# Performance work log

Hardware: AMD Instinct MI355X
Metric: run time of the kernel (lower is better)

Reference implementation:

```python
import jax, jax.numpy as jnp
import numpy as np
from jax import lax

BATCH, SEQ_LEN, INPUT_DIM, OUTPUT_DIM = 64, 1000, 512, 512
KERNEL_WIDTH = 5  # context [-2, 2] with full_context=True -> range(-2, 3)


def setup_inputs() -> dict:
    key = jax.random.key(0)
    k1, k2, k3 = jax.random.split(key, 3)
    stdv = 1.0 / np.sqrt(INPUT_DIM)
    x = jax.random.normal(k1, (BATCH, SEQ_LEN, INPUT_DIM), dtype=jnp.float32)
    kernel = stdv * jax.random.normal(k2, (OUTPUT_DIM, INPUT_DIM, KERNEL_WIDTH), dtype=jnp.float32)
    bias = stdv * jax.random.normal(k3, (OUTPUT_DIM,), dtype=jnp.float32)
    return {"x": x, "kernel": kernel, "bias": bias}


def reference(x, kernel, bias):
    # x: [B, T, C_in] -> [B, C_in, T]
    xt = jnp.transpose(x, (0, 2, 1))
    # Contiguous full context == single VALID conv over time.
    # Original loop: for each valid step i, gather x[:, :, context+i] and conv1d,
    # which for context=range(-2,3) is exactly this strided convolution.
    out = lax.conv_general_dilated(
        xt, kernel,
        window_strides=(1,), padding="VALID",
        dimension_numbers=("NCH", "OIH", "NCH"),
    )  # [B, C_out, T - K + 1]
    out = out + bias[None, :, None]
    # ReLU then transpose back to [B, T_valid, C_out]
    return jnp.transpose(jax.nn.relu(out), (0, 2, 1))
```

## Files before the change

### kernel.cpp

```cpp
#include <hip/hip_runtime.h>
#include <hip/hip_bf16.h>


#define BATCH 64
#define SEQ   1000
#define CIN   512
#define COUT  512
#define TOUT  996
#define KTOT  2560
#define MTOT  63744
#define NKT   40
#define MT    249
#define NT    2
#define NWG   (MT*NT)

typedef __bf16 bf16x8 __attribute__((ext_vector_type(8)));
typedef float  f32x4  __attribute__((ext_vector_type(4)));

__device__ __forceinline__ void gload_lds16(const void* g, void* l) {
  __builtin_amdgcn_global_load_lds(
      (const __attribute__((address_space(1))) void*)g,
      (__attribute__((address_space(3))) void*)l, 16, 0, 0);
}

#define BAR()    __builtin_amdgcn_s_barrier()
#define VM12()   asm volatile("s_waitcnt vmcnt(12)" ::: "memory")
#define VM8()    asm volatile("s_waitcnt vmcnt(8)"  ::: "memory")
#define VM4()    asm volatile("s_waitcnt vmcnt(4)"  ::: "memory")
#define PRIO(x)  __builtin_amdgcn_s_setprio(x)
#define SCHED0() __builtin_amdgcn_sched_barrier(0)
#define MFMA(d, x, y) d = __builtin_amdgcn_mfma_f32_16x16x32_bf16(x, y, d, 0, 0, 0)

__global__ void cvt_x_kernel(const float* __restrict__ x, __bf16* __restrict__ xb, int n) {
  int i = (blockIdx.x * blockDim.x + threadIdx.x) * 8;
  if (i >= n) return;
  float4 f0 = *(const float4*)(x + i);
  float4 f1 = *(const float4*)(x + i + 4);
  bf16x8 v;
  v[0] = (__bf16)f0.x; v[1] = (__bf16)f0.y; v[2] = (__bf16)f0.z; v[3] = (__bf16)f0.w;
  v[4] = (__bf16)f1.x; v[5] = (__bf16)f1.y; v[6] = (__bf16)f1.z; v[7] = (__bf16)f1.w;
  *(bf16x8*)(xb + i) = v;
}

__global__ void cvt_w_kernel(const float* __restrict__ k, __bf16* __restrict__ wt) {
  int idx = blockIdx.x * blockDim.x + threadIdx.x;
  if (idx >= 80 * 32 * 512) return;
  int j  = idx & 7;
  int l  = (idx >> 3) & 63;
  int t1 = idx >> 9;
  int ob = t1 & 31;
  int ks = t1 >> 5;
  int o  = ob * 16 + (l & 15);
  int kk = ks * 32 + ((l >> 4) & 3) * 8 + j;
  int c  = kk & 511, kw = kk >> 9;
  wt[idx] = (__bf16)k[(o * CIN + c) * 5 + kw];
}

#define STAGE(buf, kt) do { \
    char* d_ = (char*)Ab + ((buf) << 15); \
    gload_lds16(Xb + offA0 + (kt) * 64, d_ + dof0); \
    gload_lds16(Xb + offA1 + (kt) * 64, d_ + dof1); \
    gload_lds16(Xb + offA2 + (kt) * 64, d_ + dof2); \
    gload_lds16(Xb + offA3 + (kt) * 64, d_ + dof3); } while (0)

#define LOADB(bn, Tn) do { \
    const char* p_ = Wglob + (size_t)(Tn) * 65536; \
    bn[0][0] = *(const bf16x8*)(p_ +     0); bn[0][1] = *(const bf16x8*)(p_ + 32768); \
    bn[1][0] = *(const bf16x8*)(p_ +  1024); bn[1][1] = *(const bf16x8*)(p_ + 33792); \
    bn[2][0] = *(const bf16x8*)(p_ +  2048); bn[2][1] = *(const bf16x8*)(p_ + 34816); \
    bn[3][0] = *(const bf16x8*)(p_ +  3072); bn[3][1] = *(const bf16x8*)(p_ + 35840); } while (0)

#define TILE(T, bc, bn) do { \
    const bool s1_ = (T) + 1 < NKT, s2_ = (T) + 2 < NKT; \
    if (s1_) LOADB(bn, (T) + 1); \
    if (s2_) STAGE(((T) + 2) & 3, (T) + 2); \
    const char* Ac_ = Aw + (((T) & 3) << 15); \
    bf16x8 a_[4][2]; \
    _Pragma("unroll") \
    for (int mi = 0; mi < 4; ++mi) { \
      a_[mi][0] = *(const bf16x8*)(Ac_ + mi * 2048 + off0); \
      a_[mi][1] = *(const bf16x8*)(Ac_ + mi * 2048 + off1); \
    } \
    PRIO(1); \
    _Pragma("unroll") \
    for (int mi = 0; mi < 4; ++mi) \
      _Pragma("unroll") \
      for (int nj = 0; nj < 4; ++nj) { \
        MFMA(acc[mi][nj], a_[mi][0], bc[nj][0]); \
        MFMA(acc[mi][nj], a_[mi][1], bc[nj][1]); \
      } \
    PRIO(0); \
    _Pragma("unroll") \
    for (int mi = 0; mi < 4; ++mi) { \
      a_[mi][0] = *(const bf16x8*)(Ac_ + (mi + 4) * 2048 + off0); \
      a_[mi][1] = *(const bf16x8*)(Ac_ + (mi + 4) * 2048 + off1); \
    } \
    PRIO(1); \
    _Pragma("unroll") \
    for (int mi = 0; mi < 4; ++mi) \
      _Pragma("unroll") \
      for (int nj = 0; nj < 4; ++nj) { \
        MFMA(acc[mi + 4][nj], a_[mi][0], bc[nj][0]); \
        MFMA(acc[mi + 4][nj], a_[mi][1], bc[nj][1]); \
      } \
    PRIO(0); \
    SCHED0(); \
    if (s2_) { VM12(); } else if (s1_) { VM8(); } \
    if (s1_) BAR(); \
  } while (0)

__global__ __launch_bounds__(512, 2)
void tdnn_gemm_kernel(const __bf16* __restrict__ Xb, const __bf16* __restrict__ Wt2,
                      const float* __restrict__ bias, float* __restrict__ out) {
  __shared__ __bf16 Ab[4][256][64];

  const int tid  = threadIdx.x;
  const int wave = tid >> 6;
  const int lane = tid & 63;
  const int wr = wave >> 2;
  const int wc = wave & 3;

  int bid = blockIdx.x;
  int xcd = bid & 7, jj = bid >> 3;
  const int q = NWG >> 3, r = NWG & 7;
  int swz = (xcd < r ? xcd * (q + 1) : r * (q + 1) + (xcd - r) * q) + jj;
  const int m0 = (swz >> 1) * 256;
  const int n0 = (swz & 1) * 256;

  int offA0, offA1, offA2, offA3, dof0, dof1, dof2, dof3;
  {
    int o16, row, ce, m, b, tt;
#define MKOFF(l, A, D) \
    o16 = (l) * 512 + tid; row = o16 >> 3; \
    ce  = ((((o16 & 7) << 4) ^ ((row & 7) << 4)) >> 1); \
    D   = o16 * 16; \
    m = m0 + row; b = m / TOUT; tt = m - b * TOUT; \
    A = (b * SEQ + tt) * CIN + ce;
    MKOFF(0, offA0, dof0)
    MKOFF(1, offA1, dof1)
    MKOFF(2, offA2, dof2)
    MKOFF(3, offA3, dof3)
#undef MKOFF
  }

  const int frow = lane & 15;
  const int fkb  = (lane >> 4) << 4;
  const int xorv = (frow & 7) << 4;
  const int off0 = fkb ^ xorv;
  const int off1 = (64 + fkb) ^ xorv;
  const char* Aw = (const char*)Ab + (wr * 128 + frow) * 128;

  const int obW = (n0 >> 4) + wc * 4;
  const char* Wglob = (const char*)Wt2 + obW * 1024 + lane * 16;

  f32x4 acc[8][4];
  const f32x4 z = {0.f, 0.f, 0.f, 0.f};
#pragma unroll
  for (int i = 0; i < 8; i++)
#pragma unroll
    for (int j = 0; j < 4; j++) acc[i][j] = z;

  bf16x8 bA[4][2], bB[4][2];

  LOADB(bA, 0);
  STAGE(0, 0);
  STAGE(1, 1);
  VM4();
  BAR();

  for (int T = 0; T < NKT; T += 2) {
    TILE(T,     bA, bB);
    TILE(T + 1, bB, bA);
  }

  const int ccol = lane & 15;
  const int crow = (lane >> 4) * 4;
  float bv[4];
#pragma unroll
  for (int nj = 0; nj < 4; ++nj)
    bv[nj] = bias[n0 + wc * 64 + nj * 16 + ccol];

#pragma unroll
  for (int mi = 0; mi < 8; ++mi) {
    const int mrow = m0 + wr * 128 + mi * 16 + crow;
#pragma unroll
    for (int nj = 0; nj < 4; ++nj) {
      const int ocol = n0 + wc * 64 + nj * 16 + ccol;
#pragma unroll
      for (int j = 0; j < 4; ++j) {
        float v = acc[mi][nj][j] + bv[nj];
        v = v > 0.f ? v : 0.f;
        out[(size_t)(mrow + j) * COUT + ocol] = v;
      }
    }
  }
}

extern "C" void kernel_launch(void* const* d_in, const int* in_sizes, int n_in,
                              void* d_out, int out_size, void* d_ws, size_t ws_size,
                              hipStream_t stream) {
  const float* x      = (const float*)d_in[0];
  const float* kernel = (const float*)d_in[1];
  const float* bias   = (const float*)d_in[2];
  float* out          = (float*)d_out;

  __bf16* xb  = (__bf16*)d_ws;
  __bf16* wt2 = (__bf16*)((char*)d_ws + (size_t)BATCH * SEQ * CIN * 2);

  const int nx = BATCH * SEQ * CIN;
  cvt_x_kernel<<<nx / 8 / 256, 256, 0, stream>>>(x, xb, nx);
  cvt_w_kernel<<<(80 * 32 * 512 + 255) / 256, 256, 0, stream>>>(kernel, wt2);
  tdnn_gemm_kernel<<<NWG, 512, 0, stream>>>(xb, wt2, bias, out);
}
```

Before: 201.1 us.

## Stage weights through LDS and split each K-tile into barrier-synced quadrants

Weights are now converted to a plain row-major [COUT][KTOT] bf16 layout and staged into LDS with direct global-to-LDS loads, replacing the earlier per-lane register prefetch from a fragment-packed layout. The A buffer drops from four stages to two, and a two-stage B buffer is added. Each K-tile's 8x4 MFMA block is split into four quadrants, with LDS reads, async stages and barriers interleaved between them in a ping-pong schedule. The aim is to cut per-wave global B traffic and VGPR pressure and to spread memory issue across the compute phases. The cost is many more barriers per tile and a shallower prefetch depth.

```diff
diff --git a/kernel.cpp b/kernel.cpp
--- a/kernel.cpp
+++ b/kernel.cpp
@@ -24,11 +24,11 @@
 }
 
 #define BAR()    __builtin_amdgcn_s_barrier()
-#define VM12()   asm volatile("s_waitcnt vmcnt(12)" ::: "memory")
-#define VM8()    asm volatile("s_waitcnt vmcnt(8)"  ::: "memory")
-#define VM4()    asm volatile("s_waitcnt vmcnt(4)"  ::: "memory")
+#define VM6()    asm volatile("s_waitcnt vmcnt(6)" ::: "memory")
+#define VM0()    asm volatile("s_waitcnt vmcnt(0)" ::: "memory")
+#define LGKM0()  asm volatile("s_waitcnt lgkmcnt(0)" ::: "memory")
+#define LGKM8()  asm volatile("s_waitcnt lgkmcnt(8)" ::: "memory")
 #define PRIO(x)  __builtin_amdgcn_s_setprio(x)
-#define SCHED0() __builtin_amdgcn_sched_barrier(0)
 #define MFMA(d, x, y) d = __builtin_amdgcn_mfma_f32_16x16x32_bf16(x, y, d, 0, 0, 0)
 
 __global__ void cvt_x_kernel(const float* __restrict__ x, __bf16* __restrict__ xb, int n) {
@@ -44,75 +44,50 @@
 
 __global__ void cvt_w_kernel(const float* __restrict__ k, __bf16* __restrict__ wt) {
   int idx = blockIdx.x * blockDim.x + threadIdx.x;
-  if (idx >= 80 * 32 * 512) return;
-  int j  = idx & 7;
-  int l  = (idx >> 3) & 63;
-  int t1 = idx >> 9;
-  int ob = t1 & 31;
-  int ks = t1 >> 5;
-  int o  = ob * 16 + (l & 15);
-  int kk = ks * 32 + ((l >> 4) & 3) * 8 + j;
-  int c  = kk & 511, kw = kk >> 9;
+  if (idx >= COUT * KTOT) return;
+  int o  = idx / KTOT;
+  int r  = idx - o * KTOT;
+  int kw = r >> 9;
+  int c  = r & 511;
   wt[idx] = (__bf16)k[(o * CIN + c) * 5 + kw];
 }
 
-#define STAGE(buf, kt) do { \
+#define STAGE_AH(buf, h, kt) do { \
     char* d_ = (char*)Ab + ((buf) << 15); \
-    gload_lds16(Xb + offA0 + (kt) * 64, d_ + dof0); \
-    gload_lds16(Xb + offA1 + (kt) * 64, d_ + dof1); \
-    gload_lds16(Xb + offA2 + (kt) * 64, d_ + dof2); \
-    gload_lds16(Xb + offA3 + (kt) * 64, d_ + dof3); } while (0)
-
-#define LOADB(bn, Tn) do { \
-    const char* p_ = Wglob + (size_t)(Tn) * 65536; \
-    bn[0][0] = *(const bf16x8*)(p_ +     0); bn[0][1] = *(const bf16x8*)(p_ + 32768); \
-    bn[1][0] = *(const bf16x8*)(p_ +  1024); bn[1][1] = *(const bf16x8*)(p_ + 33792); \
-    bn[2][0] = *(const bf16x8*)(p_ +  2048); bn[2][1] = *(const bf16x8*)(p_ + 34816); \
-    bn[3][0] = *(const bf16x8*)(p_ +  3072); bn[3][1] = *(const bf16x8*)(p_ + 35840); } while (0)
-
-#define TILE(T, bc, bn) do { \
-    const bool s1_ = (T) + 1 < NKT, s2_ = (T) + 2 < NKT; \
-    if (s1_) LOADB(bn, (T) + 1); \
-    if (s2_) STAGE(((T) + 2) & 3, (T) + 2); \
-    const char* Ac_ = Aw + (((T) & 3) << 15); \
-    bf16x8 a_[4][2]; \
+    gload_lds16(Xb + offA##h##0 + (kt) * 64, d_ + dstA##h##0); \
+    gload_lds16(Xb + offA##h##1 + (kt) * 64, d_ + dstA##h##1); } while (0)
+#define STAGE_BH(buf, h, kt) do { \
+    char* d_ = (char*)Bb + ((buf) << 15); \
+    gload_lds16(Wt + offB##h##0 + (kt) * 64, d_ + dstB##h##0); \
+    gload_lds16(Wt + offB##h##1 + (kt) * 64, d_ + dstB##h##1); } while (0)
+
+#define RDA4(dst, base, mi0) do { \
     _Pragma("unroll") \
-    for (int mi = 0; mi < 4; ++mi) { \
-      a_[mi][0] = *(const bf16x8*)(Ac_ + mi * 2048 + off0); \
-      a_[mi][1] = *(const bf16x8*)(Ac_ + mi * 2048 + off1); \
-    } \
+    for (int mi_ = 0; mi_ < 4; ++mi_) { \
+      dst[mi_][0] = *(const bf16x8*)((base) + ((mi0) + mi_) * 2048 + off0); \
+      dst[mi_][1] = *(const bf16x8*)((base) + ((mi0) + mi_) * 2048 + off1); } } while (0)
+#define RDB2(dst, base, nj0) do { \
+    _Pragma("unroll") \
+    for (int nj_ = 0; nj_ < 2; ++nj_) { \
+      dst[nj_][0] = *(const bf16x8*)((base) + ((nj0) + nj_) * 2048 + off0); \
+      dst[nj_][1] = *(const bf16x8*)((base) + ((nj0) + nj_) * 2048 + off1); } } while (0)
+
+#define QUAD(r0, c0, AF, BF) do { \
     PRIO(1); \
     _Pragma("unroll") \
-    for (int mi = 0; mi < 4; ++mi) \
+    for (int mi_ = 0; mi_ < 4; ++mi_) \
       _Pragma("unroll") \
-      for (int nj = 0; nj < 4; ++nj) { \
-        MFMA(acc[mi][nj], a_[mi][0], bc[nj][0]); \
-        MFMA(acc[mi][nj], a_[mi][1], bc[nj][1]); \
+      for (int nj_ = 0; nj_ < 2; ++nj_) { \
+        MFMA(acc[(r0) + mi_][(c0) + nj_], AF[mi_][0], BF[nj_][0]); \
+        MFMA(acc[(r0) + mi_][(c0) + nj_], AF[mi_][1], BF[nj_][1]); \
       } \
-    PRIO(0); \
-    _Pragma("unroll") \
-    for (int mi = 0; mi < 4; ++mi) { \
-      a_[mi][0] = *(const bf16x8*)(Ac_ + (mi + 4) * 2048 + off0); \
-      a_[mi][1] = *(const bf16x8*)(Ac_ + (mi + 4) * 2048 + off1); \
-    } \
-    PRIO(1); \
-    _Pragma("unroll") \
-    for (int mi = 0; mi < 4; ++mi) \
-      _Pragma("unroll") \
-      for (int nj = 0; nj < 4; ++nj) { \
-        MFMA(acc[mi + 4][nj], a_[mi][0], bc[nj][0]); \
-        MFMA(acc[mi + 4][nj], a_[mi][1], bc[nj][1]); \
-      } \
-    PRIO(0); \
-    SCHED0(); \
-    if (s2_) { VM12(); } else if (s1_) { VM8(); } \
-    if (s1_) BAR(); \
-  } while (0)
+    PRIO(0); } while (0)
 
 __global__ __launch_bounds__(512, 2)
-void tdnn_gemm_kernel(const __bf16* __restrict__ Xb, const __bf16* __restrict__ Wt2,
+void tdnn_gemm_kernel(const __bf16* __restrict__ Xb, const __bf16* __restrict__ Wt,
                       const float* __restrict__ bias, float* __restrict__ out) {
-  __shared__ __bf16 Ab[4][256][64];
+  __shared__ __bf16 Ab[2][256][64];
+  __shared__ __bf16 Bb[2][256][64];
 
   const int tid  = threadIdx.x;
   const int wave = tid >> 6;
@@ -127,20 +102,33 @@
   const int m0 = (swz >> 1) * 256;
   const int n0 = (swz & 1) * 256;
 
-  int offA0, offA1, offA2, offA3, dof0, dof1, dof2, dof3;
+  const int tq = tid >> 3;
+  const int t8 = tid & 7;
+  const int ce = (t8 ^ (tq & 7)) << 3;
+
+  int offA00, offA01, offA10, offA11, dstA00, dstA01, dstA10, dstA11;
+  int offB00, offB01, offB10, offB11, dstB00, dstB01, dstB10, dstB11;
   {
-    int o16, row, ce, m, b, tt;
-#define MKOFF(l, A, D) \
-    o16 = (l) * 512 + tid; row = o16 >> 3; \
-    ce  = ((((o16 & 7) << 4) ^ ((row & 7) << 4)) >> 1); \
-    D   = o16 * 16; \
-    m = m0 + row; b = m / TOUT; tt = m - b * TOUT; \
-    A = (b * SEQ + tt) * CIN + ce;
-    MKOFF(0, offA0, dof0)
-    MKOFF(1, offA1, dof1)
-    MKOFF(2, offA2, dof2)
-    MKOFF(3, offA3, dof3)
-#undef MKOFF
+    int rr, m, b, tt;
+#define MKA(h, l, A, D) \
+    rr = (h) * 64 + (l) * 128 + tq; \
+    m = m0 + rr; b = m / TOUT; tt = m - b * TOUT; \
+    A = (b * SEQ + tt) * CIN + ce; \
+    D = rr * 128 + (t8 << 4);
+    MKA(0, 0, offA00, dstA00)
+    MKA(0, 1, offA01, dstA01)
+    MKA(1, 0, offA10, dstA10)
+    MKA(1, 1, offA11, dstA11)
+#undef MKA
+#define MKB(h, l, B, D) \
+    rr = (h) * 32 + ((l) * 2 + (tid >> 8)) * 64 + (tq & 31); \
+    B = (n0 + rr) * KTOT + ce; \
+    D = rr * 128 + (t8 << 4);
+    MKB(0, 0, offB00, dstB00)
+    MKB(0, 1, offB01, dstB01)
+    MKB(1, 0, offB10, dstB10)
+    MKB(1, 1, offB11, dstB11)
+#undef MKB
   }
 
   const int frow = lane & 15;
@@ -148,10 +136,8 @@
   const int xorv = (frow & 7) << 4;
   const int off0 = fkb ^ xorv;
   const int off1 = (64 + fkb) ^ xorv;
-  const char* Aw = (const char*)Ab + (wr * 128 + frow) * 128;
-
-  const int obW = (n0 >> 4) + wc * 4;
-  const char* Wglob = (const char*)Wt2 + obW * 1024 + lane * 16;
+  const char* Ab0 = (const char*)Ab + (wr * 128 + frow) * 128;
+  const char* Bb0 = (const char*)Bb + (wc * 64 + frow) * 128;
 
   f32x4 acc[8][4];
   const f32x4 z = {0.f, 0.f, 0.f, 0.f};
@@ -160,17 +146,69 @@
 #pragma unroll
     for (int j = 0; j < 4; j++) acc[i][j] = z;
 
-  bf16x8 bA[4][2], bB[4][2];
-
-  LOADB(bA, 0);
-  STAGE(0, 0);
-  STAGE(1, 1);
-  VM4();
+  bf16x8 a03[4][2], a47[4][2], b01[2][2], b23[2][2];
+
+  STAGE_AH(0, 0, 0); STAGE_AH(0, 1, 0);
+  STAGE_BH(0, 0, 0); STAGE_BH(0, 1, 0);
+  STAGE_AH(1, 0, 1); STAGE_AH(1, 1, 1);
+  STAGE_BH(1, 0, 1);
+  VM6();
   BAR();
 
-  for (int T = 0; T < NKT; T += 2) {
-    TILE(T,     bA, bB);
-    TILE(T + 1, bB, bA);
+  for (int T0 = 0; T0 < NKT; T0 += 2) {
+    const int T1 = T0 + 1;
+    const bool s2a = (T0 + 2 < NKT);
+    const bool s2b = (T1 + 2 < NKT);
+    const char* Ac = Ab0;
+    const char* Bc = Bb0;
+    const char* Ao = Ab0 + 32768;
+    const char* Bo = Bb0 + 32768;
+
+    RDA4(a03, Ac, 0); RDB2(b01, Bc, 0);
+    STAGE_BH(1, 1, T1);
+    LGKM8(); BAR(); LGKM0();
+    QUAD(0, 0, a03, b01);
+    BAR();
+
+    RDA4(a47, Ac, 4);
+    if (s2a) STAGE_AH(0, 0, T0 + 2);
+    BAR(); LGKM0();
+    QUAD(4, 0, a47, b01);
+    BAR();
+
+    RDB2(b23, Bc, 2);
+    if (s2a) STAGE_AH(0, 1, T0 + 2);
+    BAR(); LGKM0();
+    QUAD(0, 2, a03, b23);
+    BAR();
+
+    if (s2a) { STAGE_BH(0, 0, T0 + 2); VM6(); } else { VM0(); }
+    BAR();
+    QUAD(4, 2, a47, b23);
+    BAR();
+
+    RDA4(a03, Ao, 0); RDB2(b01, Bo, 0);
+    if (s2a) STAGE_BH(0, 1, T0 + 2);
+    LGKM8(); BAR(); LGKM0();
+    QUAD(0, 0, a03, b01);
+    BAR();
+
+    RDA4(a47, Ao, 4);
+    if (s2b) STAGE_AH(1, 0, T1 + 2);
+    BAR(); LGKM0();
+    QUAD(4, 0, a47, b01);
+    BAR();
+
+    RDB2(b23, Bo, 2);
+    if (s2b) STAGE_AH(1, 1, T1 + 2);
+    BAR(); LGKM0();
+    QUAD(0, 2, a03, b23);
+    BAR();
+
+    if (s2b) { STAGE_BH(1, 0, T1 + 2); VM6(); }
+    BAR();
+    QUAD(4, 2, a47, b23);
+    BAR();
   }
 
   const int ccol = lane & 15;
@@ -204,11 +242,11 @@
   const float* bias   = (const float*)d_in[2];
   float* out          = (float*)d_out;
 
-  __bf16* xb  = (__bf16*)d_ws;
-  __bf16* wt2 = (__bf16*)((char*)d_ws + (size_t)BATCH * SEQ * CIN * 2);
+  __bf16* xb = (__bf16*)d_ws;
+  __bf16* wt = (__bf16*)((char*)d_ws + (size_t)BATCH * SEQ * CIN * 2);
 
   const int nx = BATCH * SEQ * CIN;
   cvt_x_kernel<<<nx / 8 / 256, 256, 0, stream>>>(x, xb, nx);
-  cvt_w_kernel<<<(80 * 32 * 512 + 255) / 256, 256, 0, stream>>>(kernel, wt2);
-  tdnn_gemm_kernel<<<NWG, 512, 0, stream>>>(xb, wt2, bias, out);
-}
+  cvt_w_kernel<<<(COUT * KTOT + 255) / 256, 256, 0, stream>>>(kernel, wt);
+  tdnn_gemm_kernel<<<NWG, 512, 0, stream>>>(xb, wt, bias, out);
+}
```

New measurement: 202.0 us. About the same (+0.5%).
